# Kernel optimization log

Hardware: AMD Instinct MI355X
Metric: run time of the kernel (lower is better)

Reference implementation:

```python
import jax, jax.numpy as jnp
import numpy as np

HEADS = 16
DIM_HEAD = 64
SCALE = DIM_HEAD ** (-0.5)


def setup_inputs() -> dict:
    key = jax.random.key(0)
    ks = jax.random.split(key, 6)
    B, N, D = 2, 2048, 1024
    inner = HEADS * DIM_HEAD  # 1024
    s = 0.02
    return {
        "x": jax.random.normal(ks[0], (B, N, D), dtype=jnp.float32),
        "Wq": jax.random.normal(ks[1], (D, inner), dtype=jnp.float32) * s,
        "Wk": jax.random.normal(ks[2], (D, inner), dtype=jnp.float32) * s,
        "Wv": jax.random.normal(ks[3], (D, inner), dtype=jnp.float32) * s,
        "Wo": jax.random.normal(ks[4], (inner, D), dtype=jnp.float32) * s,
        "bo": jnp.zeros((D,), dtype=jnp.float32),
    }


def reference(x, Wq, Wk, Wv, Wo, bo):
    B, N, _ = x.shape
    # projections, split heads: [B, N, inner] -> [B, H, N, d]
    def split(t):
        return t.reshape(B, N, HEADS, DIM_HEAD).transpose(0, 2, 1, 3)
    q = split(x @ Wq)
    k = split(x @ Wk)  # self-attention: context = x
    v = split(x @ Wv)
    # scores [B, H, N, N], softmax over keys
    scores = jnp.einsum('bhid,bhjd->bhij', q, k) * SCALE
    attn = jax.nn.softmax(scores, axis=-1)
    out = jnp.einsum('bhij,bhjd->bhid', attn, v)
    out = out.transpose(0, 2, 1, 3).reshape(B, N, HEADS * DIM_HEAD)
    return out @ Wo + bo
```

## Files before the change

### kernel.cpp

```cpp
#include <hip/hip_runtime.h>
#include <hip/hip_bf16.h>
#include <stdint.h>

typedef unsigned short u16;
typedef __attribute__((ext_vector_type(8))) short bf16x8;
typedef __attribute__((ext_vector_type(4))) float f32x4;
typedef __attribute__((ext_vector_type(4))) unsigned int u32x4;

#define QSCALE 0.18033688011112042f

__device__ __forceinline__ u16 f2bf(float f) {
  return __builtin_bit_cast(u16, __float2bfloat16(f));
}

__device__ __forceinline__ uint32_t pkcvt(float a, float b) {
  return (uint32_t)f2bf(a) | ((uint32_t)f2bf(b) << 16);
}

__device__ __forceinline__ void gll16(const void* g, void* l) {
  __builtin_amdgcn_global_load_lds(
      (__attribute__((address_space(1))) void*)(uintptr_t)g,
      (__attribute__((address_space(3))) void*)l, 16, 0, 0);
}

__global__ __launch_bounds__(256)
void cvt_all_kernel(const float* __restrict__ x,
                    const float* __restrict__ Wq, const float* __restrict__ Wk,
                    const float* __restrict__ Wv, const float* __restrict__ Wo,
                    u16* __restrict__ xb, u16* __restrict__ Wqkvt, u16* __restrict__ Wot) {
  __shared__ float tile[32][33];
  const int bid = blockIdx.x, tid = threadIdx.x;
  if (bid < 4096) {
    const int z = bid >> 10, xy = bid & 1023;
    const float* src = (z == 0) ? Wq : (z == 1) ? Wk : (z == 2) ? Wv : Wo;
    const float scale = (z == 0) ? QSCALE : 1.0f;
    u16* dst = (z == 3) ? Wot : (Wqkvt + (size_t)z * 1024 * 1024);
    const int n0 = (xy & 31) * 32, k0 = (xy >> 5) * 32;
    const int tx = tid & 31, ty = tid >> 5;
#pragma unroll
    for (int i = 0; i < 4; ++i)
      tile[ty * 4 + i][tx] = src[(size_t)(k0 + ty * 4 + i) * 1024 + n0 + tx];
    __syncthreads();
#pragma unroll
    for (int i = 0; i < 4; ++i)
      dst[(size_t)(n0 + ty * 4 + i) * 1024 + k0 + tx] = f2bf(tile[tx][ty * 4 + i] * scale);
  } else {
    size_t i = (size_t)(bid - 4096) * 256 + tid;
    const float4* p = (const float4*)x + i * 2;
    float4 a = p[0], b = p[1];
    ushort4 lo, hi;
    lo.x = f2bf(a.x); lo.y = f2bf(a.y); lo.z = f2bf(a.z); lo.w = f2bf(a.w);
    hi.x = f2bf(b.x); hi.y = f2bf(b.y); hi.z = f2bf(b.z); hi.w = f2bf(b.w);
    ((ushort4*)xb)[i * 2]     = lo;
    ((ushort4*)xb)[i * 2 + 1] = hi;
  }
}

__global__ __launch_bounds__(512, 4)
void gemm_qkv_kernel(const u16* __restrict__ A, const u16* __restrict__ Bt,
                     u16* __restrict__ Qb, u16* __restrict__ Kb, u16* __restrict__ Vtb) {
  __shared__ __align__(16) u16 As[2][128 * 64];
  __shared__ __align__(16) u16 Bs[2][128 * 64];
  const int row0 = blockIdx.x * 128, col0 = blockIdx.y * 128;
  const int tid = threadIdx.x, lane = tid & 63, wid = tid >> 6;
  const int wr = (wid >> 2) * 64, wc = (wid & 3) * 32;
  const int lr = lane & 15, lg = lane >> 4;
  const int swz = (lr & 7) << 4;

  f32x4 acc[4][2];
#pragma unroll
  for (int m = 0; m < 4; ++m)
#pragma unroll
    for (int n = 0; n < 2; ++n) acc[m][n] = (f32x4){0.f, 0.f, 0.f, 0.f};

  auto stage = [&](int b, int k0) {
#pragma unroll
    for (int i = 0; i < 2; ++i) {
      const int c = tid + i * 512;
      const int row = c >> 3;
      const int sp = ((c & 7) * 16) ^ ((row & 7) << 4);
      gll16((const char*)A  + ((size_t)(row0 + row) * 1024 + k0) * 2 + sp, (char*)As[b] + c * 16);
      gll16((const char*)Bt + ((size_t)(col0 + row) * 1024 + k0) * 2 + sp, (char*)Bs[b] + c * 16);
    }
  };

  stage(0, 0);
  asm volatile("s_waitcnt vmcnt(0)" ::: "memory");
  __syncthreads();

  int buf = 0;
  for (int t = 0; t < 16; ++t) {
    if (t < 15) stage(buf ^ 1, (t + 1) * 64);
#pragma unroll
    for (int u = 0; u < 2; ++u) {
      const int xo = (u * 64 + lg * 16) ^ swz;
      bf16x8 af[4], bfr[2];
#pragma unroll
      for (int m = 0; m < 4; ++m)
        af[m] = *(const bf16x8*)((const char*)As[buf] + (wr + m * 16 + lr) * 128 + xo);
#pragma unroll
      for (int n = 0; n < 2; ++n)
        bfr[n] = *(const bf16x8*)((const char*)Bs[buf] + (wc + n * 16 + lr) * 128 + xo);
#pragma unroll
      for (int m = 0; m < 4; ++m)
#pragma unroll
        for (int n = 0; n < 2; ++n)
          acc[m][n] = __builtin_amdgcn_mfma_f32_16x16x32_bf16(af[m], bfr[n], acc[m][n], 0, 0, 0);
    }
    asm volatile("s_waitcnt vmcnt(0)" ::: "memory");
    __syncthreads();
    buf ^= 1;
  }

#pragma unroll
  for (int m = 0; m < 4; ++m) {
#pragma unroll
    for (int n = 0; n < 2; ++n) {
      const int gcol = col0 + wc + n * 16 + lr;
      const int w = gcol >> 10, rem = gcol & 1023;
      const int h = rem >> 6, dd = rem & 63;
      const int grow0 = row0 + wr + m * 16 + lg * 4;
      if (w == 2) {
        const int b0 = grow0 >> 11, nn0 = grow0 & 2047;
        const int kin = nn0 & 63;
        const int kp = (kin & 32) | ((kin & 12) << 1) | ((kin & 16) >> 2);
        ushort4 sv;
        sv.x = f2bf(acc[m][n][0]); sv.y = f2bf(acc[m][n][1]);
        sv.z = f2bf(acc[m][n][2]); sv.w = f2bf(acc[m][n][3]);
        *(ushort4*)&Vtb[((size_t)(b0 * 16 + h) * 64 + dd) * 2048 + (nn0 & ~63) + kp] = sv;
      } else {
#pragma unroll
        for (int r = 0; r < 4; ++r) {
          const int grow = grow0 + r;
          const int b = grow >> 11, nn = grow & 2047;
          const int bh = b * 16 + h;
          const u16 hv = f2bf(acc[m][n][r]);
          if (w == 0) Qb[((size_t)bh * 2048 + nn) * 64 + dd] = hv;
          else        Kb[((size_t)bh * 2048 + nn) * 64 + dd] = hv;
        }
      }
    }
  }
}

__global__ __launch_bounds__(256, 2)
void attn_kernel(const u16* __restrict__ Qb, const u16* __restrict__ Kb,
                 const u16* __restrict__ Vtb, u16* __restrict__ Ob) {
  __shared__ __align__(16) u16 Ks[2][128 * 64];
  __shared__ __align__(16) u16 Vs[2][128 * 64];
  const int tid = threadIdx.x, lane = tid & 63, wid = tid >> 6;
  const int bid = blockIdx.x;
  const int vv = (bid & 7) * 64 + (bid >> 3);
  const int qt = vv & 15, bh = vv >> 4;
  const int lr = lane & 15, lg = lane >> 4;

  const u16* Qp = Qb + ((size_t)bh * 2048 + qt * 128 + wid * 32) * 64;
  const char* Kg = (const char*)(Kb + (size_t)bh * 2048 * 64);
  const char* Vg = (const char*)(Vtb + (size_t)bh * 64 * 2048);

  bf16x8 aq[2][2];
#pragma unroll
  for (int qc = 0; qc < 2; ++qc)
#pragma unroll
    for (int ks = 0; ks < 2; ++ks)
      aq[qc][ks] = *(const bf16x8*)&Qp[(qc * 16 + lr) * 64 + ks * 32 + lg * 8];

  auto stage = [&](int buf, int kv0) {
#pragma unroll
    for (int i = 0; i < 4; ++i) {
      const int c = tid + i * 256;
      const int row = c >> 3;
      const int sc = ((c & 7) * 16) ^ ((row & 7) << 4);
      gll16(Kg + (size_t)(kv0 + row) * 128 + sc, (char*)Ks[buf] + c * 16);
      gll16(Vg + (size_t)(row & 63) * 4096 + (size_t)(kv0 + (row >> 6) * 64) * 2 + sc,
            (char*)Vs[buf] + c * 16);
    }
  };

  const int swz = (lr & 7) << 4;
  const int xk0 = (lg * 16) ^ swz;
  const int xk1 = (64 + lg * 16) ^ swz;

  f32x4 acco[4][2];
#pragma unroll
  for (int ct = 0; ct < 4; ++ct)
#pragma unroll
    for (int qc = 0; qc < 2; ++qc) acco[ct][qc] = (f32x4){0.f, 0.f, 0.f, 0.f};
  f32x4 lacc[2];
  lacc[0] = (f32x4){0.f, 0.f, 0.f, 0.f};
  lacc[1] = (f32x4){0.f, 0.f, 0.f, 0.f};
  const f32x4 minit = (f32x4){-8.f, -8.f, -8.f, -8.f};
  u32x4 ow;
  ow.x = ow.y = ow.z = ow.w = 0x3F803F80u;
  const bf16x8 ones = __builtin_bit_cast(bf16x8, ow);

  stage(0, 0);
  asm volatile("s_waitcnt vmcnt(0)" ::: "memory");
  __syncthreads();

  int buf = 0;
  for (int t = 0; t < 16; ++t) {
    if (t < 15) stage(buf ^ 1, (t + 1) * 128);
#pragma unroll
    for (int u = 0; u < 2; ++u) {
      const char* kbase = (const char*)Ks[buf] + u * 8192 + lr * 128;
      const char* vbase = (const char*)Vs[buf] + u * 8192 + lr * 128;

      bf16x8 kf[4][2];
#pragma unroll
      for (int kt = 0; kt < 4; ++kt) {
        kf[kt][0] = *(const bf16x8*)(kbase + kt * 2048 + xk0);
        kf[kt][1] = *(const bf16x8*)(kbase + kt * 2048 + xk1);
      }
      f32x4 s[4][2];
      __builtin_amdgcn_s_setprio(1);
#pragma unroll
      for (int kt = 0; kt < 4; ++kt)
#pragma unroll
        for (int qc = 0; qc < 2; ++qc) {
          f32x4 tacc = __builtin_amdgcn_mfma_f32_16x16x32_bf16(kf[kt][0], aq[qc][0], minit, 0, 0, 0);
          s[kt][qc]  = __builtin_amdgcn_mfma_f32_16x16x32_bf16(kf[kt][1], aq[qc][1], tacc, 0, 0, 0);
        }
      __builtin_amdgcn_s_setprio(0);
      bf16x8 pa[2][2];
#pragma unroll
      for (int qc = 0; qc < 2; ++qc) {
#pragma unroll
        for (int kt = 0; kt < 4; ++kt)
#pragma unroll
          for (int r = 0; r < 4; ++r)
            s[kt][qc][r] = __builtin_amdgcn_exp2f(s[kt][qc][r]);
#pragma unroll
        for (int ks = 0; ks < 2; ++ks) {
          u32x4 w;
          w.x = pkcvt(s[2 * ks][qc][0],     s[2 * ks][qc][1]);
          w.y = pkcvt(s[2 * ks][qc][2],     s[2 * ks][qc][3]);
          w.z = pkcvt(s[2 * ks + 1][qc][0], s[2 * ks + 1][qc][1]);
          w.w = pkcvt(s[2 * ks + 1][qc][2], s[2 * ks + 1][qc][3]);
          pa[qc][ks] = __builtin_bit_cast(bf16x8, w);
        }
        lacc[qc] = __builtin_amdgcn_mfma_f32_16x16x32_bf16(ones, pa[qc][0], lacc[qc], 0, 0, 0);
        lacc[qc] = __builtin_amdgcn_mfma_f32_16x16x32_bf16(ones, pa[qc][1], lacc[qc], 0, 0, 0);
      }
      __builtin_amdgcn_s_setprio(1);
#pragma unroll
      for (int ct = 0; ct < 4; ++ct) {
        const char* vb = vbase + ct * 2048;
#pragma unroll
        for (int ks = 0; ks < 2; ++ks) {
          bf16x8 vf = *(const bf16x8*)(vb + ((ks * 64 + lg * 16) ^ swz));
#pragma unroll
          for (int qc = 0; qc < 2; ++qc)
            acco[ct][qc] = __builtin_amdgcn_mfma_f32_16x16x32_bf16(vf, pa[qc][ks], acco[ct][qc], 0, 0, 0);
        }
      }
      __builtin_amdgcn_s_setprio(0);
    }
    asm volatile("s_waitcnt vmcnt(0)" ::: "memory");
    __syncthreads();
    buf ^= 1;
  }

  const int b = bh >> 4, h = bh & 15;
#pragma unroll
  for (int qc = 0; qc < 2; ++qc) {
    const int q = qt * 128 + wid * 32 + qc * 16 + lr;
    const float inv = 1.0f / lacc[qc][0];
#pragma unroll
    for (int ct = 0; ct < 4; ++ct) {
      uint2 st;
      st.x = pkcvt(acco[ct][qc][0] * inv, acco[ct][qc][1] * inv);
      st.y = pkcvt(acco[ct][qc][2] * inv, acco[ct][qc][3] * inv);
      *(uint2*)&Ob[((size_t)b * 2048 + q) * 1024 + h * 64 + ct * 16 + lg * 4] = st;
    }
  }
}

__global__ __launch_bounds__(512, 4)
void gemm_out_kernel(const u16* __restrict__ A, const u16* __restrict__ Bt,
                     const float* __restrict__ bo, float* __restrict__ out) {
  __shared__ __align__(16) u16 As[2][128 * 64];
  __shared__ __align__(16) u16 Bs[2][128 * 64];
  const int row0 = blockIdx.x * 128, col0 = blockIdx.y * 128;
  const int tid = threadIdx.x, lane = tid & 63, wid = tid >> 6;
  const int wr = (wid >> 2) * 64, wc = (wid & 3) * 32;
  const int lr = lane & 15, lg = lane >> 4;
  const int swz = (lr & 7) << 4;

  f32x4 acc[4][2];
#pragma unroll
  for (int m = 0; m < 4; ++m)
#pragma unroll
    for (int n = 0; n < 2; ++n) acc[m][n] = (f32x4){0.f, 0.f, 0.f, 0.f};

  auto stage = [&](int b, int k0) {
#pragma unroll
    for (int i = 0; i < 2; ++i) {
      const int c = tid + i * 512;
      const int row = c >> 3;
      const int sp = ((c & 7) * 16) ^ ((row & 7) << 4);
      gll16((const char*)A  + ((size_t)(row0 + row) * 1024 + k0) * 2 + sp, (char*)As[b] + c * 16);
      gll16((const char*)Bt + ((size_t)(col0 + row) * 1024 + k0) * 2 + sp, (char*)Bs[b] + c * 16);
    }
  };

  stage(0, 0);
  asm volatile("s_waitcnt vmcnt(0)" ::: "memory");
  __syncthreads();

  int buf = 0;
  for (int t = 0; t < 16; ++t) {
    if (t < 15) stage(buf ^ 1, (t + 1) * 64);
#pragma unroll
    for (int u = 0; u < 2; ++u) {
      const int xo = (u * 64 + lg * 16) ^ swz;
      bf16x8 af[4], bfr[2];
#pragma unroll
      for (int m = 0; m < 4; ++m)
        af[m] = *(const bf16x8*)((const char*)As[buf] + (wr + m * 16 + lr) * 128 + xo);
#pragma unroll
      for (int n = 0; n < 2; ++n)
        bfr[n] = *(const bf16x8*)((const char*)Bs[buf] + (wc + n * 16 + lr) * 128 + xo);
#pragma unroll
      for (int m = 0; m < 4; ++m)
#pragma unroll
        for (int n = 0; n < 2; ++n)
          acc[m][n] = __builtin_amdgcn_mfma_f32_16x16x32_bf16(af[m], bfr[n], acc[m][n], 0, 0, 0);
    }
    asm volatile("s_waitcnt vmcnt(0)" ::: "memory");
    __syncthreads();
    buf ^= 1;
  }

#pragma unroll
  for (int m = 0; m < 4; ++m) {
#pragma unroll
    for (int n = 0; n < 2; ++n) {
      const int gcol = col0 + wc + n * 16 + lr;
      const float bv = bo[gcol];
#pragma unroll
      for (int r = 0; r < 4; ++r) {
        const int grow = row0 + wr + m * 16 + lg * 4 + r;
        out[(size_t)grow * 1024 + gcol] = acc[m][n][r] + bv;
      }
    }
  }
}

extern "C" void kernel_launch(void* const* d_in, const int* in_sizes, int n_in,
                              void* d_out, int out_size, void* d_ws, size_t ws_size,
                              hipStream_t stream) {
  const float* x  = (const float*)d_in[0];
  const float* Wq = (const float*)d_in[1];
  const float* Wk = (const float*)d_in[2];
  const float* Wv = (const float*)d_in[3];
  const float* Wo = (const float*)d_in[4];
  const float* bo = (const float*)d_in[5];
  float* out = (float*)d_out;

  char* ws = (char*)d_ws;
  u16* xb    = (u16*)(ws);
  u16* wqkvt = (u16*)(ws + ((size_t)8  << 20));
  u16* wot   = (u16*)(ws + ((size_t)14 << 20));
  u16* Qb    = (u16*)(ws + ((size_t)16 << 20));
  u16* Kb    = (u16*)(ws + ((size_t)24 << 20));
  u16* Vtb   = (u16*)(ws + ((size_t)32 << 20));
  u16* Ob    = xb;

  hipLaunchKernelGGL(cvt_all_kernel, dim3(6144), dim3(256), 0, stream,
                     x, Wq, Wk, Wv, Wo, xb, wqkvt, wot);
  hipLaunchKernelGGL(gemm_qkv_kernel, dim3(32, 24), dim3(512), 0, stream,
                     xb, wqkvt, Qb, Kb, Vtb);
  hipLaunchKernelGGL(attn_kernel, dim3(512), dim3(256), 0, stream,
                     Qb, Kb, Vtb, Ob);
  hipLaunchKernelGGL(gemm_out_kernel, dim3(32, 8), dim3(512), 0, stream,
                     Ob, wot, bo, out);
}
```

Before: 107.3 us.

## Interleave QK and PV halves in attention loop; halve output GEMM row tile

The attention inner loop is manually unrolled so both halves' QK^T score MFMAs are issued before the first half's softmax and PV. V fragments are also loaded ahead of the exp work, giving the scheduler more independent MFMA and LDS work to overlap. Separately, the output projection GEMM drops to 64-row tiles, doubling the grid to 512 blocks so more CUs are busy, at the cost of less B-tile reuse per block. The attention change raises register pressure because both score tiles are live at once.

```diff
diff --git a/kernel.cpp b/kernel.cpp
--- a/kernel.cpp
+++ b/kernel.cpp
@@ -201,61 +201,114 @@
   int buf = 0;
   for (int t = 0; t < 16; ++t) {
     if (t < 15) stage(buf ^ 1, (t + 1) * 128);
-#pragma unroll
-    for (int u = 0; u < 2; ++u) {
-      const char* kbase = (const char*)Ks[buf] + u * 8192 + lr * 128;
-      const char* vbase = (const char*)Vs[buf] + u * 8192 + lr * 128;
-
-      bf16x8 kf[4][2];
-#pragma unroll
-      for (int kt = 0; kt < 4; ++kt) {
-        kf[kt][0] = *(const bf16x8*)(kbase + kt * 2048 + xk0);
-        kf[kt][1] = *(const bf16x8*)(kbase + kt * 2048 + xk1);
-      }
-      f32x4 s[4][2];
-      __builtin_amdgcn_s_setprio(1);
+    const char* kb0 = (const char*)Ks[buf] + lr * 128;
+    const char* kb1 = kb0 + 8192;
+    const char* vb0 = (const char*)Vs[buf] + lr * 128;
+    const char* vb1 = vb0 + 8192;
+
+    bf16x8 kf0[4][2];
+#pragma unroll
+    for (int kt = 0; kt < 4; ++kt) {
+      kf0[kt][0] = *(const bf16x8*)(kb0 + kt * 2048 + xk0);
+      kf0[kt][1] = *(const bf16x8*)(kb0 + kt * 2048 + xk1);
+    }
+    f32x4 s0[4][2];
+    __builtin_amdgcn_s_setprio(1);
+#pragma unroll
+    for (int kt = 0; kt < 4; ++kt)
+#pragma unroll
+      for (int qc = 0; qc < 2; ++qc) {
+        f32x4 tacc = __builtin_amdgcn_mfma_f32_16x16x32_bf16(kf0[kt][0], aq[qc][0], minit, 0, 0, 0);
+        s0[kt][qc] = __builtin_amdgcn_mfma_f32_16x16x32_bf16(kf0[kt][1], aq[qc][1], tacc, 0, 0, 0);
+      }
+    __builtin_amdgcn_s_setprio(0);
+    bf16x8 kf1[4][2];
+#pragma unroll
+    for (int kt = 0; kt < 4; ++kt) {
+      kf1[kt][0] = *(const bf16x8*)(kb1 + kt * 2048 + xk0);
+      kf1[kt][1] = *(const bf16x8*)(kb1 + kt * 2048 + xk1);
+    }
+    f32x4 s1[4][2];
+    __builtin_amdgcn_s_setprio(1);
+#pragma unroll
+    for (int kt = 0; kt < 4; ++kt)
+#pragma unroll
+      for (int qc = 0; qc < 2; ++qc) {
+        f32x4 tacc = __builtin_amdgcn_mfma_f32_16x16x32_bf16(kf1[kt][0], aq[qc][0], minit, 0, 0, 0);
+        s1[kt][qc] = __builtin_amdgcn_mfma_f32_16x16x32_bf16(kf1[kt][1], aq[qc][1], tacc, 0, 0, 0);
+      }
+    __builtin_amdgcn_s_setprio(0);
+    bf16x8 vf0[4][2];
+#pragma unroll
+    for (int ct = 0; ct < 4; ++ct)
+#pragma unroll
+      for (int ks = 0; ks < 2; ++ks)
+        vf0[ct][ks] = *(const bf16x8*)(vb0 + ct * 2048 + ((ks * 64 + lg * 16) ^ swz));
+    bf16x8 pa0[2][2];
+#pragma unroll
+    for (int qc = 0; qc < 2; ++qc) {
 #pragma unroll
       for (int kt = 0; kt < 4; ++kt)
 #pragma unroll
-        for (int qc = 0; qc < 2; ++qc) {
-          f32x4 tacc = __builtin_amdgcn_mfma_f32_16x16x32_bf16(kf[kt][0], aq[qc][0], minit, 0, 0, 0);
-          s[kt][qc]  = __builtin_amdgcn_mfma_f32_16x16x32_bf16(kf[kt][1], aq[qc][1], tacc, 0, 0, 0);
-        }
-      __builtin_amdgcn_s_setprio(0);
-      bf16x8 pa[2][2];
-#pragma unroll
-      for (int qc = 0; qc < 2; ++qc) {
-#pragma unroll
-        for (int kt = 0; kt < 4; ++kt)
-#pragma unroll
-          for (int r = 0; r < 4; ++r)
-            s[kt][qc][r] = __builtin_amdgcn_exp2f(s[kt][qc][r]);
-#pragma unroll
-        for (int ks = 0; ks < 2; ++ks) {
-          u32x4 w;
-          w.x = pkcvt(s[2 * ks][qc][0],     s[2 * ks][qc][1]);
-          w.y = pkcvt(s[2 * ks][qc][2],     s[2 * ks][qc][3]);
-          w.z = pkcvt(s[2 * ks + 1][qc][0], s[2 * ks + 1][qc][1]);
-          w.w = pkcvt(s[2 * ks + 1][qc][2], s[2 * ks + 1][qc][3]);
-          pa[qc][ks] = __builtin_bit_cast(bf16x8, w);
-        }
-        lacc[qc] = __builtin_amdgcn_mfma_f32_16x16x32_bf16(ones, pa[qc][0], lacc[qc], 0, 0, 0);
-        lacc[qc] = __builtin_amdgcn_mfma_f32_16x16x32_bf16(ones, pa[qc][1], lacc[qc], 0, 0, 0);
-      }
-      __builtin_amdgcn_s_setprio(1);
-#pragma unroll
-      for (int ct = 0; ct < 4; ++ct) {
-        const char* vb = vbase + ct * 2048;
-#pragma unroll
-        for (int ks = 0; ks < 2; ++ks) {
-          bf16x8 vf = *(const bf16x8*)(vb + ((ks * 64 + lg * 16) ^ swz));
-#pragma unroll
-          for (int qc = 0; qc < 2; ++qc)
-            acco[ct][qc] = __builtin_amdgcn_mfma_f32_16x16x32_bf16(vf, pa[qc][ks], acco[ct][qc], 0, 0, 0);
-        }
-      }
-      __builtin_amdgcn_s_setprio(0);
-    }
+        for (int r = 0; r < 4; ++r)
+          s0[kt][qc][r] = __builtin_amdgcn_exp2f(s0[kt][qc][r]);
+#pragma unroll
+      for (int ks = 0; ks < 2; ++ks) {
+        u32x4 w;
+        w.x = pkcvt(s0[2 * ks][qc][0],     s0[2 * ks][qc][1]);
+        w.y = pkcvt(s0[2 * ks][qc][2],     s0[2 * ks][qc][3]);
+        w.z = pkcvt(s0[2 * ks + 1][qc][0], s0[2 * ks + 1][qc][1]);
+        w.w = pkcvt(s0[2 * ks + 1][qc][2], s0[2 * ks + 1][qc][3]);
+        pa0[qc][ks] = __builtin_bit_cast(bf16x8, w);
+      }
+      lacc[qc] = __builtin_amdgcn_mfma_f32_16x16x32_bf16(ones, pa0[qc][0], lacc[qc], 0, 0, 0);
+      lacc[qc] = __builtin_amdgcn_mfma_f32_16x16x32_bf16(ones, pa0[qc][1], lacc[qc], 0, 0, 0);
+    }
+    __builtin_amdgcn_s_setprio(1);
+#pragma unroll
+    for (int ct = 0; ct < 4; ++ct)
+#pragma unroll
+      for (int ks = 0; ks < 2; ++ks)
+#pragma unroll
+        for (int qc = 0; qc < 2; ++qc)
+          acco[ct][qc] = __builtin_amdgcn_mfma_f32_16x16x32_bf16(vf0[ct][ks], pa0[qc][ks], acco[ct][qc], 0, 0, 0);
+    __builtin_amdgcn_s_setprio(0);
+    bf16x8 vf1[4][2];
+#pragma unroll
+    for (int ct = 0; ct < 4; ++ct)
+#pragma unroll
+      for (int ks = 0; ks < 2; ++ks)
+        vf1[ct][ks] = *(const bf16x8*)(vb1 + ct * 2048 + ((ks * 64 + lg * 16) ^ swz));
+    bf16x8 pa1[2][2];
+#pragma unroll
+    for (int qc = 0; qc < 2; ++qc) {
+#pragma unroll
+      for (int kt = 0; kt < 4; ++kt)
+#pragma unroll
+        for (int r = 0; r < 4; ++r)
+          s1[kt][qc][r] = __builtin_amdgcn_exp2f(s1[kt][qc][r]);
+#pragma unroll
+      for (int ks = 0; ks < 2; ++ks) {
+        u32x4 w;
+        w.x = pkcvt(s1[2 * ks][qc][0],     s1[2 * ks][qc][1]);
+        w.y = pkcvt(s1[2 * ks][qc][2],     s1[2 * ks][qc][3]);
+        w.z = pkcvt(s1[2 * ks + 1][qc][0], s1[2 * ks + 1][qc][1]);
+        w.w = pkcvt(s1[2 * ks + 1][qc][2], s1[2 * ks + 1][qc][3]);
+        pa1[qc][ks] = __builtin_bit_cast(bf16x8, w);
+      }
+      lacc[qc] = __builtin_amdgcn_mfma_f32_16x16x32_bf16(ones, pa1[qc][0], lacc[qc], 0, 0, 0);
+      lacc[qc] = __builtin_amdgcn_mfma_f32_16x16x32_bf16(ones, pa1[qc][1], lacc[qc], 0, 0, 0);
+    }
+    __builtin_amdgcn_s_setprio(1);
+#pragma unroll
+    for (int ct = 0; ct < 4; ++ct)
+#pragma unroll
+      for (int ks = 0; ks < 2; ++ks)
+#pragma unroll
+        for (int qc = 0; qc < 2; ++qc)
+          acco[ct][qc] = __builtin_amdgcn_mfma_f32_16x16x32_bf16(vf1[ct][ks], pa1[qc][ks], acco[ct][qc], 0, 0, 0);
+    __builtin_amdgcn_s_setprio(0);
+
     asm volatile("s_waitcnt vmcnt(0)" ::: "memory");
     __syncthreads();
     buf ^= 1;
@@ -279,27 +332,32 @@
 __global__ __launch_bounds__(512, 4)
 void gemm_out_kernel(const u16* __restrict__ A, const u16* __restrict__ Bt,
                      const float* __restrict__ bo, float* __restrict__ out) {
-  __shared__ __align__(16) u16 As[2][128 * 64];
+  __shared__ __align__(16) u16 As[2][64 * 64];
   __shared__ __align__(16) u16 Bs[2][128 * 64];
-  const int row0 = blockIdx.x * 128, col0 = blockIdx.y * 128;
+  const int row0 = blockIdx.x * 64, col0 = blockIdx.y * 128;
   const int tid = threadIdx.x, lane = tid & 63, wid = tid >> 6;
-  const int wr = (wid >> 2) * 64, wc = (wid & 3) * 32;
+  const int wr = (wid >> 2) * 32, wc = (wid & 3) * 32;
   const int lr = lane & 15, lg = lane >> 4;
   const int swz = (lr & 7) << 4;
 
-  f32x4 acc[4][2];
-#pragma unroll
-  for (int m = 0; m < 4; ++m)
+  f32x4 acc[2][2];
+#pragma unroll
+  for (int m = 0; m < 2; ++m)
 #pragma unroll
     for (int n = 0; n < 2; ++n) acc[m][n] = (f32x4){0.f, 0.f, 0.f, 0.f};
 
   auto stage = [&](int b, int k0) {
+    {
+      const int c = tid;
+      const int row = c >> 3;
+      const int sp = ((c & 7) * 16) ^ ((row & 7) << 4);
+      gll16((const char*)A + ((size_t)(row0 + row) * 1024 + k0) * 2 + sp, (char*)As[b] + c * 16);
+    }
 #pragma unroll
     for (int i = 0; i < 2; ++i) {
       const int c = tid + i * 512;
       const int row = c >> 3;
       const int sp = ((c & 7) * 16) ^ ((row & 7) << 4);
-      gll16((const char*)A  + ((size_t)(row0 + row) * 1024 + k0) * 2 + sp, (char*)As[b] + c * 16);
       gll16((const char*)Bt + ((size_t)(col0 + row) * 1024 + k0) * 2 + sp, (char*)Bs[b] + c * 16);
     }
   };
@@ -314,15 +372,15 @@
 #pragma unroll
     for (int u = 0; u < 2; ++u) {
       const int xo = (u * 64 + lg * 16) ^ swz;
-      bf16x8 af[4], bfr[2];
-#pragma unroll
-      for (int m = 0; m < 4; ++m)
+      bf16x8 af[2], bfr[2];
+#pragma unroll
+      for (int m = 0; m < 2; ++m)
         af[m] = *(const bf16x8*)((const char*)As[buf] + (wr + m * 16 + lr) * 128 + xo);
 #pragma unroll
       for (int n = 0; n < 2; ++n)
         bfr[n] = *(const bf16x8*)((const char*)Bs[buf] + (wc + n * 16 + lr) * 128 + xo);
 #pragma unroll
-      for (int m = 0; m < 4; ++m)
+      for (int m = 0; m < 2; ++m)
 #pragma unroll
         for (int n = 0; n < 2; ++n)
           acc[m][n] = __builtin_amdgcn_mfma_f32_16x16x32_bf16(af[m], bfr[n], acc[m][n], 0, 0, 0);
@@ -333,7 +391,7 @@
   }
 
 #pragma unroll
-  for (int m = 0; m < 4; ++m) {
+  for (int m = 0; m < 2; ++m) {
 #pragma unroll
     for (int n = 0; n < 2; ++n) {
       const int gcol = col0 + wc + n * 16 + lr;
@@ -373,6 +431,6 @@
                      xb, wqkvt, Qb, Kb, Vtb);
   hipLaunchKernelGGL(attn_kernel, dim3(512), dim3(256), 0, stream,
                      Qb, Kb, Vtb, Ob);
-  hipLaunchKernelGGL(gemm_out_kernel, dim3(32, 8), dim3(512), 0, stream,
+  hipLaunchKernelGGL(gemm_out_kernel, dim3(64, 8), dim3(512), 0, stream,
                      Ob, wot, bo, out);
 }
```

Measured after the change: 107.2 us, median of 3. Within noise of the previous version (-0.1%).
